# Kernel optimization log

Hardware: AMD Instinct MI355X
Metric: run time of the kernel (lower is better)

Reference implementation:

```python
import jax, jax.numpy as jnp
import numpy as np

GROUP_SIZE = 128
IN_FEATURES = 8192
OUT_FEATURES = 28672
TOKENS = 32


def _dequantize(qweight, qzeros, scales):
    """ExLlama q4 dequant.
    qweight: (K//8, N) int32, 8 int4 values per word packed along k.
    qzeros:  (G, N//8) int32, 8 int4 zeros per word packed along n.
    scales:  (G, N) fp16.  g = k // GROUP_SIZE; w = s * (q - (z + 1)).
    """
    shifts = jnp.arange(8, dtype=jnp.int32) * 4
    K = qweight.shape[0] * 8
    N = qweight.shape[1]
    G = qzeros.shape[0]
    # unpack weights along k: (K//8, 8, N) -> (K, N)
    q = (qweight[:, None, :] >> shifts[None, :, None]) & 15
    q = q.reshape(K, N)
    # unpack zeros along n: (G, N//8, 8) -> (G, N)
    z = (qzeros[:, :, None] >> shifts[None, None, :]) & 15
    z = z.reshape(G, N)
    # group-wise dequant: reshape k into (G, GROUP_SIZE)
    qg = q.reshape(G, GROUP_SIZE, N).astype(jnp.float16)
    zf = (z + 1).astype(jnp.float16)[:, None, :]          # ExLlama stores zero-1
    w = (qg - zf) * scales[:, None, :]                    # (G, GS, N) fp16
    return w.reshape(K, N)


def setup_inputs() -> dict:
    key = jax.random.key(0)
    k1, k2, k3, k4, k5 = jax.random.split(key, 5)
    x = jax.random.normal(k1, (TOKENS, IN_FEATURES), dtype=jnp.float16)
    qweight = jax.random.randint(k2, (IN_FEATURES // 8, OUT_FEATURES),
                                 minval=-(2**31), maxval=2**31 - 1, dtype=jnp.int32)
    qzeros = jax.random.randint(k3, (IN_FEATURES // GROUP_SIZE, OUT_FEATURES // 8),
                                minval=-(2**31), maxval=2**31 - 1, dtype=jnp.int32)
    scales = (jax.random.uniform(k4, (IN_FEATURES // GROUP_SIZE, OUT_FEATURES),
                                 dtype=jnp.float32) * 0.01 + 0.001).astype(jnp.float16)
    bias = jax.random.normal(k5, (OUT_FEATURES,), dtype=jnp.float16)
    return {"x": x, "qweight": qweight, "qzeros": qzeros,
            "scales": scales, "bias": bias}


def reference(x, qweight, qzeros, scales, bias):
    w = _dequantize(qweight, qzeros, scales)              # (K, N) fp16
    out = jnp.matmul(x.astype(jnp.float16), w)            # (T, N)
    return out + bias
```

## Files before the change

kernel.cpp:

```cpp
#include <hip/hip_runtime.h>

#define T_TOK   32
#define KDIM    8192
#define NDIM    28672
#define NGRP    64
#define NZWORDS 3584
#define NSEG    16
#define SEGK    (KDIM / NSEG)
#define GPS     (NGRP / NSEG)
#define XROW    (SEGK + 8)

typedef _Float16 half8  __attribute__((ext_vector_type(8)));
typedef _Float16 half2v __attribute__((ext_vector_type(2)));
typedef float    f32x4  __attribute__((ext_vector_type(4)));
typedef unsigned uint4v __attribute__((ext_vector_type(4)));

__global__ __launch_bounds__(256)
void exllama_gemm_lds_atomic(const int*   __restrict__ qweight,
                             const int*   __restrict__ qzeros,
                             const float* __restrict__ scales,
                             const float* __restrict__ x,
                             const float* __restrict__ bias,
                             float*       __restrict__ out)
{
    __shared__ alignas(16) _Float16 xs[T_TOK * XROW];

    const int tid  = threadIdx.x;
    const int lane = tid & 63;
    const int wav  = tid >> 6;
    const int quad = lane >> 4;
    const int l16  = lane & 15;
    const int seg  = blockIdx.y;
    const int n0   = blockIdx.x * 256 + wav * 64;

    {
        const int kseg0 = seg * SEGK;
        #pragma unroll
        for (int it = 0; it < (T_TOK * SEGK) / (256 * 8); ++it) {
            const int e  = it * 2048 + tid * 8;
            const int t  = e >> 9;
            const int kl = e & (SEGK - 1);
            const float* xp = x + (size_t)t * KDIM + kseg0 + kl;
            f32x4 lo = *(const f32x4*)xp;
            f32x4 hi = *(const f32x4*)(xp + 4);
            uint4v u;
            #pragma unroll
            for (int j = 0; j < 4; ++j)
                u[j] = __builtin_bit_cast(unsigned,
                          __builtin_amdgcn_cvt_pkrtz(lo[j], hi[j]));
            *(uint4v*)(xs + t * XROW + kl) = u;
        }
    }
    __syncthreads();

    int nc[4];
    #pragma unroll
    for (int j = 0; j < 4; ++j) nc[j] = n0 + j * 16 + l16;

    f32x4 acc[4][2];
    #pragma unroll
    for (int j = 0; j < 4; ++j)
        #pragma unroll
        for (int m = 0; m < 2; ++m)
            acc[j][m] = (f32x4){0.f, 0.f, 0.f, 0.f};

    const int g0 = seg * GPS;

    unsigned qw[2][16];
    half2v   sp[2][4], cp[2][4];

    auto load_group = [&](int g, int b) {
        #pragma unroll
        for (int j = 0; j < 4; ++j) {
            float s  = scales[(size_t)g * NDIM + nc[j]];
            int   zw = qzeros[(size_t)g * NZWORDS + (nc[j] >> 3)];
            int   z  = (zw >> ((nc[j] & 7) * 4)) & 15;
            _Float16 sh = (_Float16)s;
            _Float16 ch = (_Float16)(float)(-(1025 + z));
            sp[b][j] = (half2v){sh, sh};
            cp[b][j] = (half2v){ch, ch};
        }
        const size_t rb = (size_t)(g * 16 + quad) * NDIM;
        #pragma unroll
        for (int c = 0; c < 4; ++c)
            #pragma unroll
            for (int j = 0; j < 4; ++j)
                qw[b][c * 4 + j] = (unsigned)qweight[rb + (size_t)(c * 4) * NDIM + nc[j]];
    };

    auto compute_group = [&](int gi, int b) {
        #pragma unroll
        for (int c = 0; c < 4; ++c) {
            const int kloc = gi * 128 + c * 32 + quad * 8;
            half8 a0 = *(const half8*)(xs + l16 * XROW + kloc);
            half8 a1 = *(const half8*)(xs + (l16 + 16) * XROW + kloc);
            #pragma unroll
            for (int j = 0; j < 4; ++j) {
                const unsigned w = qw[b][c * 4 + j];
                uint4v bu;
                #pragma unroll
                for (int i = 0; i < 4; ++i) {
                    unsigned t = ((w >> (4 * i)) & 0x000F000Fu) | 0x64006400u;
                    half2v th = __builtin_bit_cast(half2v, t);
                    half2v r  = (th + cp[b][j]) * sp[b][j];
                    bu[i] = __builtin_bit_cast(unsigned, r);
                }
                half8 bf = __builtin_bit_cast(half8, bu);
                acc[j][0] = __builtin_amdgcn_mfma_f32_16x16x32_f16(a0, bf, acc[j][0], 0, 0, 0);
                acc[j][1] = __builtin_amdgcn_mfma_f32_16x16x32_f16(a1, bf, acc[j][1], 0, 0, 0);
            }
        }
    };

    load_group(g0, 0);
    #pragma unroll 1
    for (int gi = 0; gi < GPS; gi += 2) {
        load_group(g0 + gi + 1, 1);
        compute_group(gi, 0);
        if (gi + 2 < GPS) load_group(g0 + gi + 2, 0);
        compute_group(gi + 1, 1);
    }

    #pragma unroll
    for (int j = 0; j < 4; ++j) {
        const int n  = n0 + j * 16 + l16;
        const float bb = bias[n] * (1.0f / NSEG);
        #pragma unroll
        for (int m = 0; m < 2; ++m)
            #pragma unroll
            for (int r = 0; r < 4; ++r) {
                const int t = m * 16 + quad * 4 + r;
                unsafeAtomicAdd(out + (size_t)t * NDIM + n, acc[j][m][r] + bb);
            }
    }
}

extern "C" void kernel_launch(void* const* d_in, const int* in_sizes, int n_in,
                              void* d_out, int out_size, void* d_ws, size_t ws_size,
                              hipStream_t stream)
{
    const float* x  = (const float*)d_in[0];
    const int* qweight = (const int*)d_in[1];
    const int* qzeros  = (const int*)d_in[2];
    const float* sc = (const float*)d_in[3];
    const float* bs = (const float*)d_in[4];
    float* out      = (float*)d_out;
    (void)d_ws; (void)ws_size;

    exllama_gemm_lds_atomic<<<dim3(NDIM / 256, NSEG), 256, 0, stream>>>(
        qweight, qzeros, sc, x, bs, out);
}
```

Before: 217.4 us.

## Issue all segment weight loads up front before staging x into LDS

Replaces the double-buffered per-group load/compute loop with a prologue that issues every qweight, scale and zero load for the segment's four groups into registers before the x-to-LDS staging and barrier. All group loops are fully unrolled. The aim is to put more global loads in flight at once and overlap their latency with the activation staging. The cost is higher register pressure (64 weight words plus scale/zero pairs per thread), which may reduce occupancy.

```diff
diff --git a/kernel.cpp b/kernel.cpp
--- a/kernel.cpp
+++ b/kernel.cpp
@@ -16,12 +16,12 @@
 typedef unsigned uint4v __attribute__((ext_vector_type(4)));
 
 __global__ __launch_bounds__(256)
-void exllama_gemm_lds_atomic(const int*   __restrict__ qweight,
-                             const int*   __restrict__ qzeros,
-                             const float* __restrict__ scales,
-                             const float* __restrict__ x,
-                             const float* __restrict__ bias,
-                             float*       __restrict__ out)
+void exllama_gemm_deep(const int*   __restrict__ qweight,
+                       const int*   __restrict__ qzeros,
+                       const float* __restrict__ scales,
+                       const float* __restrict__ x,
+                       const float* __restrict__ bias,
+                       float*       __restrict__ out)
 {
     __shared__ alignas(16) _Float16 xs[T_TOK * XROW];
 
@@ -32,6 +32,37 @@
     const int l16  = lane & 15;
     const int seg  = blockIdx.y;
     const int n0   = blockIdx.x * 256 + wav * 64;
+
+    int nc[4];
+    #pragma unroll
+    for (int j = 0; j < 4; ++j) nc[j] = n0 + j * 16 + l16;
+
+    const int g0 = seg * GPS;
+
+    unsigned qw[GPS][16];
+    half2v   sp[GPS][4], cp[GPS][4];
+    #pragma unroll
+    for (int g = 0; g < GPS; ++g) {
+        const size_t rb = (size_t)((g0 + g) * 16 + quad) * NDIM;
+        #pragma unroll
+        for (int c = 0; c < 4; ++c)
+            #pragma unroll
+            for (int j = 0; j < 4; ++j)
+                qw[g][c * 4 + j] = (unsigned)qweight[rb + (size_t)(c * 4) * NDIM + nc[j]];
+    }
+    #pragma unroll
+    for (int g = 0; g < GPS; ++g) {
+        #pragma unroll
+        for (int j = 0; j < 4; ++j) {
+            float s  = scales[(size_t)(g0 + g) * NDIM + nc[j]];
+            int   zw = qzeros[(size_t)(g0 + g) * NZWORDS + (nc[j] >> 3)];
+            int   z  = (zw >> ((nc[j] & 7) * 4)) & 15;
+            _Float16 sh = (_Float16)s;
+            _Float16 ch = (_Float16)(float)(-(1025 + z));
+            sp[g][j] = (half2v){sh, sh};
+            cp[g][j] = (half2v){ch, ch};
+        }
+    }
 
     {
         const int kseg0 = seg * SEGK;
@@ -53,10 +84,6 @@
     }
     __syncthreads();
 
-    int nc[4];
-    #pragma unroll
-    for (int j = 0; j < 4; ++j) nc[j] = n0 + j * 16 + l16;
-
     f32x4 acc[4][2];
     #pragma unroll
     for (int j = 0; j < 4; ++j)
@@ -64,45 +91,22 @@
         for (int m = 0; m < 2; ++m)
             acc[j][m] = (f32x4){0.f, 0.f, 0.f, 0.f};
 
-    const int g0 = seg * GPS;
-
-    unsigned qw[2][16];
-    half2v   sp[2][4], cp[2][4];
-
-    auto load_group = [&](int g, int b) {
-        #pragma unroll
-        for (int j = 0; j < 4; ++j) {
-            float s  = scales[(size_t)g * NDIM + nc[j]];
-            int   zw = qzeros[(size_t)g * NZWORDS + (nc[j] >> 3)];
-            int   z  = (zw >> ((nc[j] & 7) * 4)) & 15;
-            _Float16 sh = (_Float16)s;
-            _Float16 ch = (_Float16)(float)(-(1025 + z));
-            sp[b][j] = (half2v){sh, sh};
-            cp[b][j] = (half2v){ch, ch};
-        }
-        const size_t rb = (size_t)(g * 16 + quad) * NDIM;
-        #pragma unroll
-        for (int c = 0; c < 4; ++c)
-            #pragma unroll
-            for (int j = 0; j < 4; ++j)
-                qw[b][c * 4 + j] = (unsigned)qweight[rb + (size_t)(c * 4) * NDIM + nc[j]];
-    };
-
-    auto compute_group = [&](int gi, int b) {
+    #pragma unroll
+    for (int g = 0; g < GPS; ++g) {
         #pragma unroll
         for (int c = 0; c < 4; ++c) {
-            const int kloc = gi * 128 + c * 32 + quad * 8;
+            const int kloc = g * 128 + c * 32 + quad * 8;
             half8 a0 = *(const half8*)(xs + l16 * XROW + kloc);
             half8 a1 = *(const half8*)(xs + (l16 + 16) * XROW + kloc);
             #pragma unroll
             for (int j = 0; j < 4; ++j) {
-                const unsigned w = qw[b][c * 4 + j];
+                const unsigned w = qw[g][c * 4 + j];
                 uint4v bu;
                 #pragma unroll
                 for (int i = 0; i < 4; ++i) {
                     unsigned t = ((w >> (4 * i)) & 0x000F000Fu) | 0x64006400u;
                     half2v th = __builtin_bit_cast(half2v, t);
-                    half2v r  = (th + cp[b][j]) * sp[b][j];
+                    half2v r  = (th + cp[g][j]) * sp[g][j];
                     bu[i] = __builtin_bit_cast(unsigned, r);
                 }
                 half8 bf = __builtin_bit_cast(half8, bu);
@@ -110,15 +114,6 @@
                 acc[j][1] = __builtin_amdgcn_mfma_f32_16x16x32_f16(a1, bf, acc[j][1], 0, 0, 0);
             }
         }
-    };
-
-    load_group(g0, 0);
-    #pragma unroll 1
-    for (int gi = 0; gi < GPS; gi += 2) {
-        load_group(g0 + gi + 1, 1);
-        compute_group(gi, 0);
-        if (gi + 2 < GPS) load_group(g0 + gi + 2, 0);
-        compute_group(gi + 1, 1);
     }
 
     #pragma unroll
@@ -147,6 +142,6 @@
     float* out      = (float*)d_out;
     (void)d_ws; (void)ws_size;
 
-    exllama_gemm_lds_atomic<<<dim3(NDIM / 256, NSEG), 256, 0, stream>>>(
+    exllama_gemm_deep<<<dim3(NDIM / 256, NSEG), 256, 0, stream>>>(
         qweight, qzeros, sc, x, bs, out);
 }
```

Result: faster. 208.1 us (-4.3%).
